# Kernel tuning notes

Measured on AMD Instinct MI355X. Metric: run time of the kernel, lower is better.

Reference implementation:

```python
import jax, jax.numpy as jnp
import numpy as np

B, S, H = 8, 2048, 768

def setup_inputs() -> dict:
    key = jax.random.key(0)
    ks = jax.random.split(key, 11)
    queries = jax.random.normal(ks[0], (B, S, H), dtype=jnp.float32)
    keys_ = jax.random.normal(ks[1], (B, S, H), dtype=jnp.float32)
    values = jax.random.normal(ks[2], (B, S, H), dtype=jnp.float32)
    coordinates = jax.random.uniform(ks[3], (B, S, 2), dtype=jnp.float32)
    scale = 1.0 / np.sqrt(H)
    Wq = jax.random.normal(ks[4], (H, H), dtype=jnp.float32) * scale
    bq = jnp.zeros((H,), dtype=jnp.float32)
    Wk = jax.random.normal(ks[5], (H, H), dtype=jnp.float32) * scale
    bk = jnp.zeros((H,), dtype=jnp.float32)
    Wv = jax.random.normal(ks[6], (H, H), dtype=jnp.float32) * scale
    bv = jnp.zeros((H,), dtype=jnp.float32)
    spatial_weight = jax.random.normal(ks[7], (1,), dtype=jnp.float32)
    return {"queries": queries, "keys": keys_, "values": values,
            "coordinates": coordinates, "Wq": Wq, "bq": bq, "Wk": Wk,
            "bk": bk, "Wv": Wv, "bv": bv, "spatial_weight": spatial_weight}

def _cdist(c):
    # c: [B, S, 2] -> pairwise euclidean distances [B, S, S]
    sq = jnp.sum(c * c, axis=-1)  # [B, S]
    d2 = sq[:, :, None] + sq[:, None, :] - 2.0 * jnp.einsum('bsd,btd->bst', c, c)
    return jnp.sqrt(jnp.maximum(d2, 1e-12))

def reference(queries, keys, values, coordinates, Wq, bq, Wk, bk, Wv, bv, spatial_weight):
    q = queries @ Wq.T + bq  # [B, S, H]
    k = keys @ Wk.T + bk
    v = values @ Wv.T + bv
    scores = jnp.einsum('bsh,bth->bst', q, k)          # [B, S, S]
    scores = scores - spatial_weight[0] * _cdist(coordinates)
    attn = jax.nn.softmax(scores, axis=-1)
    out = jnp.einsum('bst,bth->bsh', attn, v)          # [B, S, H]
    return out, attn
```

## Files before the change

kernel.cpp:

```cpp
#include <hip/hip_runtime.h>
#include <stdint.h>


typedef _Float16 half8 __attribute__((ext_vector_type(8)));
typedef _Float16 half4v __attribute__((ext_vector_type(4)));
typedef float f32x4 __attribute__((ext_vector_type(4)));

#define DEVI static __device__ __forceinline__

constexpr int B_ = 8, S_ = 2048, H_ = 768;
constexpr long NX = (long)B_ * S_ * H_;
constexpr long NW = (long)H_ * H_;
constexpr long ATT = (long)B_ * S_ * S_;

DEVI void glds16(const void* g, void* l) {
  __builtin_amdgcn_global_load_lds(
      (const __attribute__((address_space(1))) uint32_t*)g,
      (__attribute__((address_space(3))) uint32_t*)l, 16, 0, 0);
}

DEVI void stage_tile(const _Float16* gbase, int rowStride, _Float16* lds, int tid) {
#pragma unroll
  for (int seg = 0; seg < 2; ++seg) {
    int u = seg * 256 + tid;
    int r = u >> 2, c = u & 3;
    int sc = c ^ ((r >> 1) & 3);
    glds16(gbase + (long)r * rowStride + sc * 8, lds + ((u & ~63) << 3));
  }
}

DEVI half8 frag(const _Float16* lds, int m0, int lane) {
  int row = m0 + (lane & 15);
  int c = (lane >> 4) ^ ((row >> 1) & 3);
  return *(const half8*)(lds + row * 32 + c * 8);
}

__global__ __launch_bounds__(256) void k_split(
    const float* __restrict__ xq, const float* __restrict__ xk,
    const float* __restrict__ xv, const float* __restrict__ wq,
    const float* __restrict__ wk, const float* __restrict__ wv,
    _Float16* __restrict__ dst) {
  const long NX4 = NX / 4, NW4 = NW / 4, TOT = 3 * NX4 + 3 * NW4;
  for (long u = (long)blockIdx.x * blockDim.x + threadIdx.x; u < TOT;
       u += (long)gridDim.x * blockDim.x) {
    const float4* src;
    _Float16 *dh, *dl;
    bool wantLo = true;
    long idx;
    if (u < 3 * NX4) {
      int z = (u >= 2 * NX4) ? 2 : (u >= NX4) ? 1 : 0;
      idx = u - (long)z * NX4;
      src = (const float4*)(z == 0 ? xq : z == 1 ? xk : xv);
      dh = dst + (long)z * 2 * NX;
      dl = dh + NX;
      wantLo = (z < 2);
    } else {
      long t = u - 3 * NX4;
      int z = (t >= 2 * NW4) ? 2 : (t >= NW4) ? 1 : 0;
      idx = t - (long)z * NW4;
      src = (const float4*)(z == 0 ? wq : z == 1 ? wk : wv);
      dh = dst + 5 * NX + (long)z * 2 * NW;
      dl = dh + NW;
      wantLo = (z < 2);
    }
    float4 x = src[idx];
    half4v hi, lo;
    hi[0] = (_Float16)x.x; lo[0] = (_Float16)(x.x - (float)hi[0]);
    hi[1] = (_Float16)x.y; lo[1] = (_Float16)(x.y - (float)hi[1]);
    hi[2] = (_Float16)x.z; lo[2] = (_Float16)(x.z - (float)hi[2]);
    hi[3] = (_Float16)x.w; lo[3] = (_Float16)(x.w - (float)hi[3]);
    *(half4v*)(dh + idx * 4) = hi;
    if (wantLo) *(half4v*)(dl + idx * 4) = lo;
  }
}

__global__ __launch_bounds__(256, 2) void k_proj(
    const _Float16* __restrict__ scratch, const float* __restrict__ bq,
    const float* __restrict__ bk, const float* __restrict__ bv,
    _Float16* __restrict__ qh, _Float16* __restrict__ ql,
    _Float16* __restrict__ kh, _Float16* __restrict__ kl,
    _Float16* __restrict__ vT) {
  const int nt = blockIdx.x, mt = blockIdx.y, z = blockIdx.z;
  const int tid = threadIdx.x;
  const bool full = (z < 2);
  const _Float16* Xh = scratch + (long)z * 2 * NX;
  const _Float16* Xl = Xh + NX;
  const _Float16* Wh = scratch + 5 * NX + (long)z * 2 * NW;
  const _Float16* Wl = Wh + NW;
  const float* bias = (z == 0) ? bq : (z == 1) ? bk : bv;

  __shared__ _Float16 sm[2][4][4096];
  f32x4 acc[4][4] = {};

  const _Float16* Ah = Xh + (long)(mt * 128) * H_;
  const _Float16* Al = Xl + (long)(mt * 128) * H_;
  const _Float16* Bh = Wh + (long)(nt * 128) * H_;
  const _Float16* Bl = Wl + (long)(nt * 128) * H_;

  stage_tile(Ah, H_, sm[0][0], tid);
  stage_tile(Bh, H_, sm[0][2], tid);
  if (full) {
    stage_tile(Al, H_, sm[0][1], tid);
    stage_tile(Bl, H_, sm[0][3], tid);
  }
  __syncthreads();

  const int lane = tid & 63, wid = tid >> 6;
  const int wm = (wid >> 1) * 64, wn = (wid & 1) * 64;

  int cur = 0;
  for (int kk = 0; kk < 24; ++kk) {
    if (kk + 1 < 24) {
      int o = (kk + 1) * 32;
      stage_tile(Ah + o, H_, sm[cur ^ 1][0], tid);
      stage_tile(Bh + o, H_, sm[cur ^ 1][2], tid);
      if (full) {
        stage_tile(Al + o, H_, sm[cur ^ 1][1], tid);
        stage_tile(Bl + o, H_, sm[cur ^ 1][3], tid);
      }
    }
    half8 ah[4], bh[4];
#pragma unroll
    for (int i = 0; i < 4; ++i) ah[i] = frag(sm[cur][0], wm + i * 16, lane);
#pragma unroll
    for (int j = 0; j < 4; ++j) bh[j] = frag(sm[cur][2], wn + j * 16, lane);
#pragma unroll
    for (int i = 0; i < 4; ++i)
#pragma unroll
      for (int j = 0; j < 4; ++j)
        acc[i][j] = __builtin_amdgcn_mfma_f32_16x16x32_f16(ah[i], bh[j],
                                                           acc[i][j], 0, 0, 0);
    if (full) {
      half8 al[4], bl[4];
#pragma unroll
      for (int i = 0; i < 4; ++i) al[i] = frag(sm[cur][1], wm + i * 16, lane);
#pragma unroll
      for (int j = 0; j < 4; ++j) bl[j] = frag(sm[cur][3], wn + j * 16, lane);
#pragma unroll
      for (int i = 0; i < 4; ++i)
#pragma unroll
        for (int j = 0; j < 4; ++j) {
          acc[i][j] = __builtin_amdgcn_mfma_f32_16x16x32_f16(ah[i], bl[j],
                                                             acc[i][j], 0, 0, 0);
          acc[i][j] = __builtin_amdgcn_mfma_f32_16x16x32_f16(al[i], bh[j],
                                                             acc[i][j], 0, 0, 0);
        }
    }
    __syncthreads();
    cur ^= 1;
  }

  _Float16* oh = (z == 0) ? qh : kh;
  _Float16* ol = (z == 0) ? ql : kl;
#pragma unroll
  for (int i = 0; i < 4; ++i) {
    int m_t = wm + i * 16 + ((lane >> 4) << 2);
#pragma unroll
    for (int j = 0; j < 4; ++j) {
      int n_t = wn + j * 16 + (lane & 15);
      int gn = nt * 128 + n_t;
      float bs = bias[gn];
      if (full) {
#pragma unroll
        for (int r = 0; r < 4; ++r) {
          long gm = (long)mt * 128 + m_t + r;
          float y = acc[i][j][r] + bs;
          _Float16 hi = (_Float16)y;
          oh[gm * H_ + gn] = hi;
          ol[gm * H_ + gn] = (_Float16)(y - (float)hi);
        }
      } else {
        int gmI = mt * 128 + m_t;
        int bb = gmI >> 11, t0 = gmI & 2047;
        half4v pk;
#pragma unroll
        for (int r = 0; r < 4; ++r) pk[r] = (_Float16)(acc[i][j][r] + bs);
        *(half4v*)&vT[((long)bb * H_ + gn) * S_ + t0] = pk;
      }
    }
  }
}

__global__ __launch_bounds__(512, 2) void k_scores8p(
    const _Float16* __restrict__ qh, const _Float16* __restrict__ ql,
    const _Float16* __restrict__ kh_, const _Float16* __restrict__ kl_,
    const float* __restrict__ coords, const float* __restrict__ sw,
    float* __restrict__ attn) {
  int bid = blockIdx.x + 8 * blockIdx.y + 64 * blockIdx.z;
  int swz = (bid & 7) * 64 + (bid >> 3);
  const int nt = swz & 7, mt = (swz >> 3) & 7, b = swz >> 6;
  const int tid = threadIdx.x, lane = tid & 63, wid = tid >> 6;
  const int wr = wid >> 2, wc = wid & 3;

  __shared__ _Float16 lds[2][2][2][8192];
  __shared__ float cco[4][256];

  if (tid < 256) {
    long gi = (long)b * S_ + mt * 256 + tid;
    cco[0][tid] = coords[gi * 2 + 0];
    cco[1][tid] = coords[gi * 2 + 1];
  } else {
    int t = tid - 256;
    long gj = (long)b * S_ + nt * 256 + t;
    cco[2][t] = coords[gj * 2 + 0];
    cco[3][t] = coords[gj * 2 + 1];
  }
  const float w = sw[0];

  const long aoff = ((long)b * S_ + mt * 256) * H_;
  const long boff = ((long)b * S_ + nt * 256) * H_;

  long goff[2];
  int loff[2];
#pragma unroll
  for (int seg = 0; seg < 2; ++seg) {
    int u = seg * 512 + tid;
    int r = u >> 2, c = u & 3;
    int sc = c ^ ((r >> 1) & 3);
    goff[seg] = (long)r * H_ + sc * 8;
    loff[seg] = (u & ~63) << 3;
  }

  f32x4 acc[8][4] = {};

  auto stage_half = [&](int h) {
    int th = h >> 2, kind = h & 3;
    int khf = kind >> 1, mx = kind & 1;
    int term = th % 3;
    long ko = (long)(th / 3) * 64 + khf * 32;
    const _Float16* src = mx ? ((term == 1 ? kl_ : kh_) + boff + ko)
                             : ((term == 2 ? ql : qh) + aoff + ko);
    _Float16* dst = &lds[th & 1][khf][mx][0];
    glds16(src + goff[0], dst + loff[0]);
    glds16(src + goff[1], dst + loff[1]);
  };

  half8 bf[4];

  auto phase = [&](int slot, int kh2, int mh, int hst, int vm) {
    const _Float16* A = &lds[slot][kh2][0][0];
    const _Float16* Bt = &lds[slot][kh2][1][0];
    half8 af[4];
    if (mh == 0) {
#pragma unroll
      for (int j = 0; j < 4; ++j) bf[j] = frag(Bt, wc * 64 + j * 16, lane);
    }
#pragma unroll
    for (int i = 0; i < 4; ++i)
      af[i] = frag(A, wr * 128 + mh * 64 + i * 16, lane);
    if (hst >= 0) stage_half(hst);
    if (vm == 6) asm volatile("s_waitcnt vmcnt(6)" ::: "memory");
    else if (vm == 0) asm volatile("s_waitcnt vmcnt(0)" ::: "memory");
    __builtin_amdgcn_s_barrier();
    asm volatile("s_waitcnt lgkmcnt(0)" ::: "memory");
    __builtin_amdgcn_sched_barrier(0);
    __builtin_amdgcn_s_setprio(1);
#pragma unroll
    for (int i = 0; i < 4; ++i)
#pragma unroll
      for (int j = 0; j < 4; ++j)
        acc[mh * 4 + i][j] = __builtin_amdgcn_mfma_f32_16x16x32_f16(
            af[i], bf[j], acc[mh * 4 + i][j], 0, 0, 0);
    __builtin_amdgcn_s_setprio(0);
    asm volatile("" ::: "memory");
    __builtin_amdgcn_s_barrier();
  };

#pragma unroll
  for (int h = 0; h < 7; ++h) stage_half(h);
  asm volatile("s_waitcnt vmcnt(6)" ::: "memory");
  __builtin_amdgcn_s_barrier();

#pragma unroll 1
  for (int t = 0; t < 34; ++t) {
    const int slot = t & 1, P = 4 * t;
    phase(slot, 0, 0, P + 7, -1);
    phase(slot, 0, 1, P + 8, -1);
    phase(slot, 1, 0, P + 9, -1);
    phase(slot, 1, 1, P + 10, 6);
  }
  phase(0, 0, 0, 143, -1);
  phase(0, 0, 1, -1, -1);
  phase(0, 1, 0, -1, -1);
  phase(0, 1, 1, -1, 0);
  phase(1, 0, 0, -1, -1);
  phase(1, 0, 1, -1, -1);
  phase(1, 1, 0, -1, -1);
  phase(1, 1, 1, -1, -1);

#pragma unroll
  for (int mi = 0; mi < 8; ++mi) {
    int m_t = wr * 128 + mi * 16 + ((lane >> 4) << 2);
#pragma unroll
    for (int j = 0; j < 4; ++j) {
      int n_t = wc * 64 + j * 16 + (lane & 15);
      float cjx = cco[2][n_t], cjy = cco[3][n_t];
      long rowbase = ((long)b * S_ + mt * 256 + m_t) * S_ + nt * 256 + n_t;
#pragma unroll
      for (int r = 0; r < 4; ++r) {
        float dx = cco[0][m_t + r] - cjx;
        float dy = cco[1][m_t + r] - cjy;
        float d = sqrtf(fmaxf(fmaf(dx, dx, dy * dy), 1e-12f));
        attn[rowbase + (long)r * S_] = acc[mi][j][r] - w * d;
      }
    }
  }
}

__global__ __launch_bounds__(256) void k_rowsoft(float* __restrict__ attn,
                                                 _Float16* __restrict__ a16) {
  const int wid = threadIdx.x >> 6, lane = threadIdx.x & 63;
  long row = (long)blockIdx.x * 4 + wid;
  float* p = attn + row * S_;
  _Float16* p16 = a16 + row * S_;
  float4 v[8];
#pragma unroll
  for (int i = 0; i < 8; ++i) v[i] = ((const float4*)p)[i * 64 + lane];
  float m = -3.4e38f;
#pragma unroll
  for (int i = 0; i < 8; ++i)
    m = fmaxf(m, fmaxf(fmaxf(v[i].x, v[i].y), fmaxf(v[i].z, v[i].w)));
#pragma unroll
  for (int o = 32; o > 0; o >>= 1) m = fmaxf(m, __shfl_xor(m, o));
  float l = 0.f;
#pragma unroll
  for (int i = 0; i < 8; ++i) {
    v[i].x = __expf(v[i].x - m);
    v[i].y = __expf(v[i].y - m);
    v[i].z = __expf(v[i].z - m);
    v[i].w = __expf(v[i].w - m);
    l += (v[i].x + v[i].y) + (v[i].z + v[i].w);
  }
#pragma unroll
  for (int o = 32; o > 0; o >>= 1) l += __shfl_xor(l, o);
  const float rl = 1.0f / l;
#pragma unroll
  for (int i = 0; i < 8; ++i) {
    v[i].x *= rl; v[i].y *= rl; v[i].z *= rl; v[i].w *= rl;
    ((float4*)p)[i * 64 + lane] = v[i];
    half4v h = {(_Float16)v[i].x, (_Float16)v[i].y, (_Float16)v[i].z,
                (_Float16)v[i].w};
    ((half4v*)p16)[i * 64 + lane] = h;
  }
}

__global__ __launch_bounds__(256, 2) void k_pv16(
    const _Float16* __restrict__ a16, const _Float16* __restrict__ vT,
    float* __restrict__ outp) {
  int bid = blockIdx.x + 6 * blockIdx.y + 96 * blockIdx.z;
  int swz = (bid & 7) * 96 + (bid >> 3);
  const int nt = swz % 6, mt = (swz / 6) & 15, b = swz / 96;
  const int tid = threadIdx.x, lane = tid & 63, wid = tid >> 6;
  const int wm = (wid >> 1) * 64, wn = (wid & 1) * 64;
  __shared__ _Float16 sm[2][2][4096];
  f32x4 acc[4][4] = {};
  const _Float16* Ab = a16 + ((long)b * S_ + mt * 128) * S_;
  const _Float16* Bb = vT + ((long)b * H_ + nt * 128) * S_;

  stage_tile(Ab, S_, sm[0][0], tid);
  stage_tile(Bb, S_, sm[0][1], tid);
  __syncthreads();

  int cur = 0;
  for (int kk = 0; kk < 64; ++kk) {
    if (kk + 1 < 64) {
      stage_tile(Ab + (kk + 1) * 32, S_, sm[cur ^ 1][0], tid);
      stage_tile(Bb + (kk + 1) * 32, S_, sm[cur ^ 1][1], tid);
    }
    half8 ah[4], bh[4];
#pragma unroll
    for (int i = 0; i < 4; ++i) ah[i] = frag(sm[cur][0], wm + i * 16, lane);
#pragma unroll
    for (int j = 0; j < 4; ++j) bh[j] = frag(sm[cur][1], wn + j * 16, lane);
#pragma unroll
    for (int i = 0; i < 4; ++i)
#pragma unroll
      for (int j = 0; j < 4; ++j)
        acc[i][j] = __builtin_amdgcn_mfma_f32_16x16x32_f16(ah[i], bh[j],
                                                           acc[i][j], 0, 0, 0);
    __syncthreads();
    cur ^= 1;
  }

#pragma unroll
  for (int i = 0; i < 4; ++i) {
    int m_t = wm + i * 16 + ((lane >> 4) << 2);
#pragma unroll
    for (int j = 0; j < 4; ++j) {
      int n_t = wn + j * 16 + (lane & 15);
      int h = nt * 128 + n_t;
      long rowbase = (long)b * S_ + mt * 128 + m_t;
#pragma unroll
      for (int r = 0; r < 4; ++r) outp[(rowbase + r) * H_ + h] = acc[i][j][r];
    }
  }
}

extern "C" void kernel_launch(void* const* d_in, const int* in_sizes, int n_in,
                              void* d_out, int out_size, void* d_ws,
                              size_t ws_size, hipStream_t stream) {
  const float* xq = (const float*)d_in[0];
  const float* xk = (const float*)d_in[1];
  const float* xv = (const float*)d_in[2];
  const float* co = (const float*)d_in[3];
  const float* wq = (const float*)d_in[4];
  const float* bq = (const float*)d_in[5];
  const float* wk = (const float*)d_in[6];
  const float* bk = (const float*)d_in[7];
  const float* wv = (const float*)d_in[8];
  const float* bv = (const float*)d_in[9];
  const float* sw = (const float*)d_in[10];

  float* out = (float*)d_out;
  float* attn = out + NX;
  _Float16* scratch = (_Float16*)d_out;

  _Float16* qh = (_Float16*)d_ws;
  _Float16* ql = qh + NX;
  _Float16* kh = ql + NX;
  _Float16* kl = kh + NX;
  _Float16* vT = kl + NX;
  _Float16* a16 = qh;

  k_split<<<dim3(2048), 256, 0, stream>>>(xq, xk, xv, wq, wk, wv, scratch);
  k_proj<<<dim3(6, 128, 3), 256, 0, stream>>>(scratch, bq, bk, bv, qh, ql, kh,
                                              kl, vT);
  k_scores8p<<<dim3(8, 8, 8), 512, 0, stream>>>(qh, ql, kh, kl, co, sw, attn);
  k_rowsoft<<<dim3(4096), 256, 0, stream>>>(attn, a16);
  k_pv16<<<dim3(6, 16, 8), 256, 0, stream>>>(a16, vT, out);
}
```

Baseline: 482.6 us.

## Fold Wq^T Wk into a single matrix to drop the K projection GEMM

Rewrites q·k as x_q (Wq^T Wk) x_k^T, computing G = Wq^T Wk once as a small 768x768 split-precision GEMM (after transposing the weights). Queries are projected by G while raw keys are used directly, which removes one of the three large B*S*H projection GEMMs. Bias terms are folded in as per-row and per-column additive vectors built by small dot-product kernels. This adds several small launches and a different rounding path through the combined matrix.

```diff
diff --git a/kernel.cpp b/kernel.cpp
--- a/kernel.cpp
+++ b/kernel.cpp
@@ -39,29 +39,28 @@
     const float* __restrict__ xq, const float* __restrict__ xk,
     const float* __restrict__ xv, const float* __restrict__ wq,
     const float* __restrict__ wk, const float* __restrict__ wv,
-    _Float16* __restrict__ dst) {
+    _Float16* __restrict__ xqh, _Float16* __restrict__ xkh,
+    _Float16* __restrict__ xvh, _Float16* __restrict__ wb) {
   const long NX4 = NX / 4, NW4 = NW / 4, TOT = 3 * NX4 + 3 * NW4;
   for (long u = (long)blockIdx.x * blockDim.x + threadIdx.x; u < TOT;
        u += (long)gridDim.x * blockDim.x) {
     const float4* src;
-    _Float16 *dh, *dl;
+    _Float16 *dh, *dl = nullptr;
     bool wantLo = true;
     long idx;
     if (u < 3 * NX4) {
       int z = (u >= 2 * NX4) ? 2 : (u >= NX4) ? 1 : 0;
       idx = u - (long)z * NX4;
-      src = (const float4*)(z == 0 ? xq : z == 1 ? xk : xv);
-      dh = dst + (long)z * 2 * NX;
-      dl = dh + NX;
-      wantLo = (z < 2);
+      if (z == 0) { src = (const float4*)xq; dh = xqh; dl = xqh + NX; }
+      else if (z == 1) { src = (const float4*)xk; dh = xkh; dl = xkh + NX; }
+      else { src = (const float4*)xv; dh = xvh; wantLo = false; }
     } else {
       long t = u - 3 * NX4;
       int z = (t >= 2 * NW4) ? 2 : (t >= NW4) ? 1 : 0;
       idx = t - (long)z * NW4;
-      src = (const float4*)(z == 0 ? wq : z == 1 ? wk : wv);
-      dh = dst + 5 * NX + (long)z * 2 * NW;
-      dl = dh + NW;
-      wantLo = (z < 2);
+      if (z == 0) { src = (const float4*)wq; dh = wb; dl = wb + NW; }
+      else if (z == 1) { src = (const float4*)wk; dh = wb + 2 * NW; dl = wb + 3 * NW; }
+      else { src = (const float4*)wv; dh = wb + 4 * NW; wantLo = false; }
     }
     float4 x = src[idx];
     half4v hi, lo;
@@ -74,20 +73,119 @@
   }
 }
 
-__global__ __launch_bounds__(256, 2) void k_proj(
-    const _Float16* __restrict__ scratch, const float* __restrict__ bq,
-    const float* __restrict__ bk, const float* __restrict__ bv,
-    _Float16* __restrict__ qh, _Float16* __restrict__ ql,
-    _Float16* __restrict__ kh, _Float16* __restrict__ kl,
-    _Float16* __restrict__ vT) {
+__global__ __launch_bounds__(256) void k_tr(const _Float16* __restrict__ in,
+                                            _Float16* __restrict__ out) {
+  const int z = blockIdx.z;
+  const _Float16* src = in + (long)z * NW;
+  _Float16* dst = out + (long)z * NW;
+  __shared__ _Float16 t[64][72];
+  int r0 = blockIdx.y * 64, c0 = blockIdx.x * 64;
+#pragma unroll
+  for (int it = 0; it < 2; ++it) {
+    int idx = it * 256 + threadIdx.x;
+    int r = idx >> 3, ch = idx & 7;
+    *(half8*)&t[r][ch * 8] = *(const half8*)(src + (long)(r0 + r) * H_ + c0 + ch * 8);
+  }
+  __syncthreads();
+#pragma unroll
+  for (int it = 0; it < 2; ++it) {
+    int idx = it * 256 + threadIdx.x;
+    int r = idx >> 3, ch = idx & 7;
+    half8 v;
+#pragma unroll
+    for (int k = 0; k < 8; ++k) v[k] = t[ch * 8 + k][r];
+    *(half8*)(dst + (long)(c0 + r) * H_ + r0 + ch * 8) = v;
+  }
+}
+
+__global__ __launch_bounds__(256, 2) void k_gemm3(
+    const _Float16* __restrict__ Ah_, const _Float16* __restrict__ Al_,
+    const _Float16* __restrict__ Bh_, const _Float16* __restrict__ Bl_,
+    _Float16* __restrict__ Oh, _Float16* __restrict__ Ol) {
+  const int nt = blockIdx.x, mt = blockIdx.y;
+  const int tid = threadIdx.x;
+  __shared__ _Float16 sm[2][4][4096];
+  f32x4 acc[4][4] = {};
+  const _Float16* Ah = Ah_ + (long)(mt * 128) * H_;
+  const _Float16* Al = Al_ + (long)(mt * 128) * H_;
+  const _Float16* Bh = Bh_ + (long)(nt * 128) * H_;
+  const _Float16* Bl = Bl_ + (long)(nt * 128) * H_;
+
+  stage_tile(Ah, H_, sm[0][0], tid);
+  stage_tile(Bh, H_, sm[0][2], tid);
+  stage_tile(Al, H_, sm[0][1], tid);
+  stage_tile(Bl, H_, sm[0][3], tid);
+  __syncthreads();
+
+  const int lane = tid & 63, wid = tid >> 6;
+  const int wm = (wid >> 1) * 64, wn = (wid & 1) * 64;
+
+  int cur = 0;
+  for (int kk = 0; kk < 24; ++kk) {
+    if (kk + 1 < 24) {
+      int o = (kk + 1) * 32;
+      stage_tile(Ah + o, H_, sm[cur ^ 1][0], tid);
+      stage_tile(Bh + o, H_, sm[cur ^ 1][2], tid);
+      stage_tile(Al + o, H_, sm[cur ^ 1][1], tid);
+      stage_tile(Bl + o, H_, sm[cur ^ 1][3], tid);
+    }
+    half8 ah[4], bh[4], al[4], bl[4];
+#pragma unroll
+    for (int i = 0; i < 4; ++i) {
+      ah[i] = frag(sm[cur][0], wm + i * 16, lane);
+      al[i] = frag(sm[cur][1], wm + i * 16, lane);
+    }
+#pragma unroll
+    for (int j = 0; j < 4; ++j) {
+      bh[j] = frag(sm[cur][2], wn + j * 16, lane);
+      bl[j] = frag(sm[cur][3], wn + j * 16, lane);
+    }
+#pragma unroll
+    for (int i = 0; i < 4; ++i)
+#pragma unroll
+      for (int j = 0; j < 4; ++j) {
+        acc[i][j] = __builtin_amdgcn_mfma_f32_16x16x32_f16(ah[i], bh[j],
+                                                           acc[i][j], 0, 0, 0);
+        acc[i][j] = __builtin_amdgcn_mfma_f32_16x16x32_f16(ah[i], bl[j],
+                                                           acc[i][j], 0, 0, 0);
+        acc[i][j] = __builtin_amdgcn_mfma_f32_16x16x32_f16(al[i], bh[j],
+                                                           acc[i][j], 0, 0, 0);
+      }
+    __syncthreads();
+    cur ^= 1;
+  }
+
+#pragma unroll
+  for (int i = 0; i < 4; ++i) {
+    int m_t = wm + i * 16 + ((lane >> 4) << 2);
+#pragma unroll
+    for (int j = 0; j < 4; ++j) {
+      int n_t = wn + j * 16 + (lane & 15);
+      int gn = nt * 128 + n_t;
+#pragma unroll
+      for (int r = 0; r < 4; ++r) {
+        long gm = (long)mt * 128 + m_t + r;
+        float y = acc[i][j][r];
+        _Float16 hi = (_Float16)y;
+        Oh[gm * H_ + gn] = hi;
+        Ol[gm * H_ + gn] = (_Float16)(y - (float)hi);
+      }
+    }
+  }
+}
+
+__global__ __launch_bounds__(256, 2) void k_gemmPV(
+    const _Float16* __restrict__ xqh, const _Float16* __restrict__ xvh,
+    const _Float16* __restrict__ gth, const _Float16* __restrict__ wvh,
+    const float* __restrict__ bv, _Float16* __restrict__ Ph,
+    _Float16* __restrict__ Pl, _Float16* __restrict__ vT) {
   const int nt = blockIdx.x, mt = blockIdx.y, z = blockIdx.z;
   const int tid = threadIdx.x;
-  const bool full = (z < 2);
-  const _Float16* Xh = scratch + (long)z * 2 * NX;
-  const _Float16* Xl = Xh + NX;
-  const _Float16* Wh = scratch + 5 * NX + (long)z * 2 * NW;
-  const _Float16* Wl = Wh + NW;
-  const float* bias = (z == 0) ? bq : (z == 1) ? bk : bv;
+  const bool full = (z == 0);
+  const _Float16* Xh = full ? xqh : xvh;
+  const _Float16* Xl = xqh + NX;
+  const _Float16* Wh = full ? gth : wvh;
+  const _Float16* Wl = gth + NW;
 
   __shared__ _Float16 sm[2][4][4096];
   f32x4 acc[4][4] = {};
@@ -150,8 +248,6 @@
     cur ^= 1;
   }
 
-  _Float16* oh = (z == 0) ? qh : kh;
-  _Float16* ol = (z == 0) ? ql : kl;
 #pragma unroll
   for (int i = 0; i < 4; ++i) {
     int m_t = wm + i * 16 + ((lane >> 4) << 2);
@@ -159,17 +255,17 @@
     for (int j = 0; j < 4; ++j) {
       int n_t = wn + j * 16 + (lane & 15);
       int gn = nt * 128 + n_t;
-      float bs = bias[gn];
       if (full) {
 #pragma unroll
         for (int r = 0; r < 4; ++r) {
           long gm = (long)mt * 128 + m_t + r;
-          float y = acc[i][j][r] + bs;
+          float y = acc[i][j][r];
           _Float16 hi = (_Float16)y;
-          oh[gm * H_ + gn] = hi;
-          ol[gm * H_ + gn] = (_Float16)(y - (float)hi);
+          Ph[gm * H_ + gn] = hi;
+          Pl[gm * H_ + gn] = (_Float16)(y - (float)hi);
         }
       } else {
+        float bs = bv[gn];
         int gmI = mt * 128 + m_t;
         int bb = gmI >> 11, t0 = gmI & 2047;
         half4v pk;
@@ -179,12 +275,50 @@
       }
     }
   }
+}
+
+__global__ __launch_bounds__(256) void k_uv(const float* __restrict__ wq,
+                                            const float* __restrict__ wk,
+                                            const float* __restrict__ bq,
+                                            const float* __restrict__ bk,
+                                            float* u, float* vv, float* cb) {
+  int i = blockIdx.x * 256 + threadIdx.x;
+  const float* W = (blockIdx.y == 0) ? wq : wk;
+  const float* bvec = (blockIdx.y == 0) ? bk : bq;
+  float a = 0;
+  for (int j = 0; j < H_; ++j) a = fmaf(W[(long)j * H_ + i], bvec[j], a);
+  ((blockIdx.y == 0) ? u : vv)[i] = a;
+  if (blockIdx.x == 0 && blockIdx.y == 0 && threadIdx.x == 0) {
+    float c = 0;
+    for (int j = 0; j < H_; ++j) c += bq[j] * bk[j];
+    cb[0] = c;
+  }
+}
+
+__global__ __launch_bounds__(256) void k_dot(const float* __restrict__ src,
+                                             const float* __restrict__ vec,
+                                             const float* __restrict__ cb,
+                                             float* __restrict__ dst, int addc) {
+  int wid = threadIdx.x >> 6, lane = threadIdx.x & 63;
+  long row = (long)blockIdx.x * 4 + wid;
+  const float4* p = (const float4*)(src + row * H_);
+  const float4* q = (const float4*)vec;
+  float s = 0;
+#pragma unroll
+  for (int k = 0; k < 3; ++k) {
+    float4 a = p[lane + k * 64], b = q[lane + k * 64];
+    s += a.x * b.x + a.y * b.y + a.z * b.z + a.w * b.w;
+  }
+#pragma unroll
+  for (int o = 32; o; o >>= 1) s += __shfl_xor(s, o);
+  if (lane == 0) dst[row] = s + (addc ? cb[0] : 0.0f);
 }
 
 __global__ __launch_bounds__(512, 2) void k_scores8p(
     const _Float16* __restrict__ qh, const _Float16* __restrict__ ql,
     const _Float16* __restrict__ kh_, const _Float16* __restrict__ kl_,
     const float* __restrict__ coords, const float* __restrict__ sw,
+    const float* __restrict__ rowadd, const float* __restrict__ coladd,
     float* __restrict__ attn) {
   int bid = blockIdx.x + 8 * blockIdx.y + 64 * blockIdx.z;
   int swz = (bid & 7) * 64 + (bid >> 3);
@@ -194,16 +328,19 @@
 
   __shared__ _Float16 lds[2][2][2][8192];
   __shared__ float cco[4][256];
+  __shared__ float rca[2][256];
 
   if (tid < 256) {
     long gi = (long)b * S_ + mt * 256 + tid;
     cco[0][tid] = coords[gi * 2 + 0];
     cco[1][tid] = coords[gi * 2 + 1];
+    rca[0][tid] = rowadd[gi];
   } else {
     int t = tid - 256;
     long gj = (long)b * S_ + nt * 256 + t;
     cco[2][t] = coords[gj * 2 + 0];
     cco[3][t] = coords[gj * 2 + 1];
+    rca[1][t] = coladd[gj];
   }
   const float w = sw[0];
 
@@ -295,13 +432,15 @@
     for (int j = 0; j < 4; ++j) {
       int n_t = wc * 64 + j * 16 + (lane & 15);
       float cjx = cco[2][n_t], cjy = cco[3][n_t];
+      float ca = rca[1][n_t];
       long rowbase = ((long)b * S_ + mt * 256 + m_t) * S_ + nt * 256 + n_t;
 #pragma unroll
       for (int r = 0; r < 4; ++r) {
         float dx = cco[0][m_t + r] - cjx;
         float dy = cco[1][m_t + r] - cjy;
         float d = sqrtf(fmaxf(fmaf(dx, dx, dy * dy), 1e-12f));
-        attn[rowbase + (long)r * S_] = acc[mi][j][r] - w * d;
+        attn[rowbase + (long)r * S_] =
+            acc[mi][j][r] - w * d + rca[0][m_t + r] + ca;
       }
     }
   }
@@ -413,19 +552,37 @@
 
   float* out = (float*)d_out;
   float* attn = out + NX;
-  _Float16* scratch = (_Float16*)d_out;
-
-  _Float16* qh = (_Float16*)d_ws;
-  _Float16* ql = qh + NX;
-  _Float16* kh = ql + NX;
-  _Float16* kl = kh + NX;
-  _Float16* vT = kl + NX;
-  _Float16* a16 = qh;
-
-  k_split<<<dim3(2048), 256, 0, stream>>>(xq, xk, xv, wq, wk, wv, scratch);
-  k_proj<<<dim3(6, 128, 3), 256, 0, stream>>>(scratch, bq, bk, bv, qh, ql, kh,
-                                              kl, vT);
-  k_scores8p<<<dim3(8, 8, 8), 512, 0, stream>>>(qh, ql, kh, kl, co, sw, attn);
+
+  _Float16* sc = (_Float16*)d_out;
+  _Float16* Xqh = sc;
+  _Float16* Xvh = sc + 2 * NX;
+  _Float16* Wbase = sc + 3 * NX;
+  _Float16* WT = Wbase + 5 * NW;
+  _Float16* GtH = Wbase + 9 * NW;
+  float* rowadd = out;
+  float* coladd = out + 16384;
+  float* u = out + 32768;
+  float* vv = u + H_;
+  float* cb = vv + H_;
+
+  _Float16* Ph = (_Float16*)d_ws;
+  _Float16* Pl = Ph + NX;
+  _Float16* Xkh = Ph + 2 * NX;
+  _Float16* vT = Ph + 4 * NX;
+  _Float16* a16 = Ph;
+
+  k_split<<<dim3(2048), 256, 0, stream>>>(xq, xk, xv, wq, wk, wv, Xqh, Xkh,
+                                          Xvh, Wbase);
+  k_tr<<<dim3(12, 12, 4), 256, 0, stream>>>(Wbase, WT);
+  k_gemm3<<<dim3(6, 6), 256, 0, stream>>>(WT + 2 * NW, WT + 3 * NW, WT,
+                                          WT + NW, GtH, GtH + NW);
+  k_gemmPV<<<dim3(6, 128, 2), 256, 0, stream>>>(Xqh, Xvh, GtH, Wbase + 4 * NW,
+                                                bv, Ph, Pl, vT);
+  k_uv<<<dim3(3, 2), 256, 0, stream>>>(wq, wk, bq, bk, u, vv, cb);
+  k_dot<<<dim3(4096), 256, 0, stream>>>(xq, u, cb, rowadd, 1);
+  k_dot<<<dim3(4096), 256, 0, stream>>>(xk, vv, cb, coladd, 0);
+  k_scores8p<<<dim3(8, 8, 8), 512, 0, stream>>>(Ph, Pl, Xkh, Xkh + NX, co, sw,
+                                                rowadd, coladd, attn);
   k_rowsoft<<<dim3(4096), 256, 0, stream>>>(attn, a16);
   k_pv16<<<dim3(6, 16, 8), 256, 0, stream>>>(a16, vT, out);
 }
```

After: 555.5 us. +15.1%, slower.
